# Performance work log

Measured on AMD Instinct MI355X. Metric: run time of the kernel, lower is better.

The kernel has to match this reference:

```python
import jax, jax.numpy as jnp
import numpy as np

HIDDEN = 64
HALF = 32
VOCAB = 64
B, L = 256, 2048


def _l2norm(x):
    # matches torch F.normalize(dim=-1, eps=1e-12)
    return x / jnp.maximum(jnp.linalg.norm(x, axis=-1, keepdims=True), 1e-12)


def setup_inputs() -> dict:
    key = jax.random.key(0)
    ks = jax.random.split(key, 16)
    s = 0.02
    return {
        "seq": jax.random.randint(ks[0], (B, L), 0, VOCAB),
        "embed": jax.random.normal(ks[1], (VOCAB, HIDDEN), jnp.float32) * s,
        "W1": jax.random.normal(ks[2], (2 * HIDDEN, HIDDEN), jnp.float32) * s,
        "b1": jnp.zeros((2 * HIDDEN,), jnp.float32),
        "W2": jax.random.normal(ks[3], (HIDDEN, 2 * HIDDEN), jnp.float32) * s,
        "b2": jnp.zeros((HIDDEN,), jnp.float32),
        "ln_g": jnp.ones((HIDDEN,), jnp.float32),
        "ln_b": jnp.zeros((HIDDEN,), jnp.float32),
        "Ws": jax.random.normal(ks[4], (HALF, HIDDEN), jnp.float32) * s,
        "bs": jnp.zeros((HALF,), jnp.float32),
        "We": jax.random.normal(ks[5], (HALF, HIDDEN), jnp.float32) * s,
        "be": jnp.zeros((HALF,), jnp.float32),
        "Wrp": jax.random.normal(ks[6], (HIDDEN, 2 * HALF), jnp.float32) * s,
        "brp": jnp.zeros((HIDDEN,), jnp.float32),
        "Wo": jax.random.normal(ks[7], (VOCAB, HIDDEN), jnp.float32) * s,
        "bo": jnp.zeros((VOCAB,), jnp.float32),
    }


def reference(seq, embed, W1, b1, W2, b2, ln_g, ln_b, Ws, bs, We, be, Wrp, brp, Wo, bo):
    # Encoder: embed -> LayerNorm(h + FF(h))
    h0 = embed[seq]                                     # [B,L,H]
    ff = jnp.maximum(h0 @ W1.T + b1, 0.0) @ W2.T + b2
    x = h0 + ff
    mu = x.mean(-1, keepdims=True)
    var = x.var(-1, keepdims=True)
    h = (x - mu) / jnp.sqrt(var + 1e-5) * ln_g + ln_b   # [B,L,H]

    Bn, Ln, _ = h.shape
    half = Ws.shape[0]
    hs_all = h @ Ws.T + bs                              # [B,L,half]
    he_all = h @ We.T + be

    # sequential delta-rule memory writes over t = 0 .. L-2
    hs_seq = jnp.swapaxes(hs_all[:, :-1], 0, 1)         # [L-1,B,half]
    he_seq = jnp.swapaxes(he_all[:, :-1], 0, 1)
    scales = (jnp.arange(1, Ln) / Ln).astype(h.dtype)   # (t+1)/L
    M0 = jnp.zeros((Bn, half, half), h.dtype)

    def step(carry, inp):
        M_s, M_e = carry
        hs, he, sc = inp
        ks_ = _l2norm(hs)
        ke_ = _l2norm(he)
        vps = jnp.einsum('bij,bj->bi', M_s, ks_)
        vpe = jnp.einsum('bij,bj->bi', M_e, ke_)
        M_s = M_s + (hs - vps)[:, :, None] * ks_[:, None, :]
        M_e = M_e + sc * (he - vpe)[:, :, None] * ke_[:, None, :]
        return (M_s, M_e), None

    (M_s, M_e), _ = jax.lax.scan(step, (M0, M0), (hs_seq, he_seq, scales))

    # read with last-position query
    qs = _l2norm(hs_all[:, -1])
    qe = _l2norm(he_all[:, -1])
    rs = jnp.einsum('bij,bj->bi', M_s, qs)
    re = jnp.einsum('bij,bj->bi', M_e, qe)
    r = jnp.concatenate([rs, re], axis=-1)              # [B, 2*half]
    return (r @ Wrp.T + brp) @ Wo.T + bo                # [B, vocab]
```

## Files before the change

### kernel.cpp

```cpp
#include <hip/hip_runtime.h>

#define HIDDEN 64
#define HALFD  32
#define VOCAB  64
#define BATCH  256
#define SEQLEN 2048
#define GPAD   65

#define RLF(v, sl) __int_as_float(__builtin_amdgcn_readlane(__float_as_int(v), (sl)))
#define RFL(x)     __builtin_amdgcn_readfirstlane(x)

__global__ __launch_bounds__(64) void vocab_kernel(
    const float* __restrict__ embed, const float* __restrict__ W1, const float* __restrict__ b1,
    const float* __restrict__ W2, const float* __restrict__ b2,
    const float* __restrict__ ln_g, const float* __restrict__ ln_b,
    const float* __restrict__ Ws, const float* __restrict__ bs,
    const float* __restrict__ We, const float* __restrict__ be,
    float* __restrict__ ws)
{
    const int v = blockIdx.x;
    const int tid = threadIdx.x;

    __shared__ float e_s[64];
    __shared__ float a1_s[128];
    __shared__ float h_s[64];

    e_s[tid] = embed[v * 64 + tid];
    __syncthreads();

    float acc0 = b1[tid], acc1 = b1[tid + 64];
    #pragma unroll 8
    for (int m = 0; m < 64; ++m) {
        float ev = e_s[m];
        acc0 = fmaf(ev, W1[tid * 64 + m], acc0);
        acc1 = fmaf(ev, W1[(tid + 64) * 64 + m], acc1);
    }
    a1_s[tid]      = fmaxf(acc0, 0.0f);
    a1_s[tid + 64] = fmaxf(acc1, 0.0f);
    __syncthreads();

    float ff = b2[tid];
    #pragma unroll 8
    for (int m = 0; m < 128; ++m) ff = fmaf(a1_s[m], W2[tid * 128 + m], ff);
    float x = e_s[tid] + ff;

    float s = x, s2 = x * x;
    #pragma unroll
    for (int off = 32; off >= 1; off >>= 1) {
        s  += __shfl_xor(s,  off, 64);
        s2 += __shfl_xor(s2, off, 64);
    }
    float mu  = s * (1.0f / 64.0f);
    float var = s2 * (1.0f / 64.0f) - mu * mu;
    float hval = (x - mu) * rsqrtf(var + 1e-5f) * ln_g[tid] + ln_b[tid];
    h_s[tid] = hval;
    __syncthreads();

    const int j = tid & 31;
    const bool is_s = tid < 32;
    const float* W = is_s ? Ws : We;
    float acc = is_s ? bs[j] : be[j];
    #pragma unroll 8
    for (int m = 0; m < 64; ++m) acc = fmaf(h_s[m], W[j * 64 + m], acc);

    float n2 = acc * acc;
    #pragma unroll
    for (int off = 16; off >= 1; off >>= 1) n2 += __shfl_xor(n2, off, 64);
    float norm = sqrtf(n2);
    float kn = acc / fmaxf(norm, 1e-12f);

    const int base = v * 32 + j;
    if (is_s) { ws[base]        = kn; ws[4096 + base] = acc; }
    else      { ws[2048 + base] = kn; ws[6144 + base] = acc; }
}

__global__ __launch_bounds__(256) void gram_kernel(float* __restrict__ ws)
{
    const int w = blockIdx.x;
    const int tid = threadIdx.x;
    __shared__ float k_s[2048];
    const float* kb = ws + w * 2048;
    for (int i = tid; i < 2048; i += 256) k_s[i] = kb[i];
    __syncthreads();
    const int a  = tid >> 2;
    const int b0 = (tid & 3) << 4;
    float* Gw = ws + 8192 + w * 4096 + a * 64;
    for (int bb = 0; bb < 16; ++bb) {
        const int bcol = b0 + bb;
        float acc = 0.f;
        #pragma unroll
        for (int m = 0; m < 32; ++m) acc = fmaf(k_s[a * 32 + m], k_s[bcol * 32 + m], acc);
        Gw[bcol] = acc;
    }
}

__global__ __launch_bounds__(128) void scan_kernel(
    const int* __restrict__ seq, const float* __restrict__ ws,
    const float* __restrict__ Wrp, const float* __restrict__ brp,
    const float* __restrict__ Wo, const float* __restrict__ bo,
    float* __restrict__ out)
{
    const int b    = blockIdx.x;
    const int tid  = threadIdx.x;
    const int w    = tid >> 6;
    const int lane = tid & 63;
    const bool is_e = (w == 1);

    __shared__ float Gl[2 * 64 * GPAD];
    __shared__ int   toklds[SEQLEN];
    __shared__ float wacc_s[2][64];
    __shared__ float r_s[64];
    __shared__ float t1_s[64];

    {
        const float4* gsrc = (const float4*)(ws + 8192);
        for (int i4 = tid; i4 < 2048; i4 += 128) {
            float4 gv = gsrc[i4];
            int idx = i4 << 2;
            int ww = idx >> 12, rc = idx & 4095;
            int rowi = rc >> 6, coli = rc & 63;
            float* d = &Gl[ww * (64 * GPAD) + rowi * GPAD + coli];
            d[0] = gv.x; d[1] = gv.y; d[2] = gv.z; d[3] = gv.w;
        }
        const int4* sq4 = (const int4*)(seq + b * SEQLEN);
        int4* tl4w = (int4*)toklds;
        #pragma unroll
        for (int i = 0; i < 4; ++i) tl4w[tid + i * 128] = sq4[tid + i * 128];
    }
    __syncthreads();

    const float* Gw = Gl + w * (64 * GPAD);
    const int4*  tl4 = (const int4*)toklds;

    const float invL = 1.0f / (float)SEQLEN;

    int4 tA  = tl4[510], tB  = tl4[511];
    int tk0 = RFL(tA.x), tk1 = RFL(tA.y), tk2 = RFL(tA.z), tk3 = RFL(tA.w);
    int tk4 = RFL(tB.x), tk5 = RFL(tB.y), tk6 = RFL(tB.z), tk7 = RFL(tB.w);
    int4 tA1 = tl4[508], tB1 = tl4[509];
    int nk0 = RFL(tA1.x), nk1 = RFL(tA1.y), nk2 = RFL(tA1.z), nk3 = RFL(tA1.w);
    int nk4 = RFL(tB1.x), nk5 = RFL(tB1.y), nk6 = RFL(tB1.z), nk7 = RFL(tB1.w);

    float grow0 = Gw[tk0 * GPAD + lane], grow1 = Gw[tk1 * GPAD + lane];
    float grow2 = Gw[tk2 * GPAD + lane], grow3 = Gw[tk3 * GPAD + lane];
    float grow4 = Gw[tk4 * GPAD + lane], grow5 = Gw[tk5 * GPAD + lane];
    float grow6 = Gw[tk6 * GPAD + lane], grow7 = Gw[tk7 * GPAD + lane];

    float u     = Gw[tk7 * GPAD + lane];
    float waccv = 0.0f;

    for (int c = 255; c >= 0; --c) {
        float t0 = __shfl(u, tk0, 64);
        float t1 = __shfl(u, tk1, 64);
        float t2 = __shfl(u, tk2, 64);
        float t3 = __shfl(u, tk3, 64);
        float t4 = __shfl(u, tk4, 64);
        float t5 = __shfl(u, tk5, 64);
        float t6 = __shfl(u, tk6, 64);
        float t7 = __shfl(u, tk7, 64);

        float g01 = RLF(grow0, tk1), g02 = RLF(grow0, tk2), g03 = RLF(grow0, tk3);
        float g04 = RLF(grow0, tk4), g05 = RLF(grow0, tk5), g06 = RLF(grow0, tk6), g07 = RLF(grow0, tk7);
        float g12 = RLF(grow1, tk2), g13 = RLF(grow1, tk3), g14 = RLF(grow1, tk4);
        float g15 = RLF(grow1, tk5), g16 = RLF(grow1, tk6), g17 = RLF(grow1, tk7);
        float g23 = RLF(grow2, tk3), g24 = RLF(grow2, tk4), g25 = RLF(grow2, tk5);
        float g26 = RLF(grow2, tk6), g27 = RLF(grow2, tk7);
        float g34 = RLF(grow3, tk4), g35 = RLF(grow3, tk5), g36 = RLF(grow3, tk6), g37 = RLF(grow3, tk7);
        float g45 = RLF(grow4, tk5), g46 = RLF(grow4, tk6), g47 = RLF(grow4, tk7);
        float g56 = RLF(grow5, tk6), g57 = RLF(grow5, tk7);
        float g67 = RLF(grow6, tk7);

        float gn0 = Gw[nk0 * GPAD + lane], gn1 = Gw[nk1 * GPAD + lane];
        float gn2 = Gw[nk2 * GPAD + lane], gn3 = Gw[nk3 * GPAD + lane];
        float gn4 = Gw[nk4 * GPAD + lane], gn5 = Gw[nk5 * GPAD + lane];
        float gn6 = Gw[nk6 * GPAD + lane], gn7 = Gw[nk7 * GPAD + lane];
        int cm2 = (c >= 2) ? (c - 2) : 0;
        int4 tA2 = tl4[cm2 * 2], tB2 = tl4[cm2 * 2 + 1];

        float fb = (float)(8 * c + 1) * invL;
        float f0 = is_e ? fb            : 1.0f;
        float f1 = is_e ? fb +     invL : 1.0f;
        float f2 = is_e ? fb + 2 * invL : 1.0f;
        float f3 = is_e ? fb + 3 * invL : 1.0f;
        float f4 = is_e ? fb + 4 * invL : 1.0f;
        float f5 = is_e ? fb + 5 * invL : 1.0f;
        float f6 = is_e ? fb + 6 * invL : 1.0f;
        float f7 = (c == 255) ? 0.0f : (is_e ? fb + 7 * invL : 1.0f);

        float s7 = f7 * t7;
        float s6 = f6 * (t6 - g67 * s7);
        float s5 = f5 * ((t5 - g57 * s7) - g56 * s6);
        float s4 = f4 * (((t4 - g47 * s7) - g46 * s6) - g45 * s5);
        float s3 = f3 * ((((t3 - g37 * s7) - g36 * s6) - g35 * s5) - g34 * s4);
        float s2 = f2 * (((((t2 - g27 * s7) - g26 * s6) - g25 * s5) - g24 * s4) - g23 * s3);
        float s1 = f1 * ((((((t1 - g17 * s7) - g16 * s6) - g15 * s5) - g14 * s4) - g13 * s3) - g12 * s2);
        float s0 = f0 * (((((((t0 - g07 * s7) - g06 * s6) - g05 * s5) - g04 * s4) - g03 * s3) - g02 * s2) - g01 * s1);

        {
            float A = fmaf(grow0, s0, fmaf(grow1, s1, fmaf(grow2, s2, grow3 * s3)));
            float B = fmaf(grow4, s4, fmaf(grow5, s5, fmaf(grow6, s6, grow7 * s7)));
            u -= (A + B);
        }

        waccv += (lane == tk0) ? s0 : 0.0f;
        waccv += (lane == tk1) ? s1 : 0.0f;
        waccv += (lane == tk2) ? s2 : 0.0f;
        waccv += (lane == tk3) ? s3 : 0.0f;
        waccv += (lane == tk4) ? s4 : 0.0f;
        waccv += (lane == tk5) ? s5 : 0.0f;
        waccv += (lane == tk6) ? s6 : 0.0f;
        waccv += (lane == tk7) ? s7 : 0.0f;

        tk0 = nk0; tk1 = nk1; tk2 = nk2; tk3 = nk3;
        tk4 = nk4; tk5 = nk5; tk6 = nk6; tk7 = nk7;
        nk0 = RFL(tA2.x); nk1 = RFL(tA2.y); nk2 = RFL(tA2.z); nk3 = RFL(tA2.w);
        nk4 = RFL(tB2.x); nk5 = RFL(tB2.y); nk6 = RFL(tB2.z); nk7 = RFL(tB2.w);
        grow0 = gn0; grow1 = gn1; grow2 = gn2; grow3 = gn3;
        grow4 = gn4; grow5 = gn5; grow6 = gn6; grow7 = gn7;
    }

    wacc_s[w][lane] = waccv;
    __syncthreads();

    if (tid < 64) {
        const int w2  = tid >> 5;
        const int rho = tid & 31;
        const float* vv = ws + 4096 + w2 * 2048;
        const float* wa = &wacc_s[w2][0];
        float acc = 0.0f;
        #pragma unroll 8
        for (int tok = 0; tok < 64; ++tok) acc = fmaf(wa[tok], vv[tok * 32 + rho], acc);
        r_s[tid] = acc;
    }
    __syncthreads();

    if (tid < 64) {
        float acc = brp[tid];
        #pragma unroll 8
        for (int m = 0; m < 64; ++m) acc = fmaf(Wrp[tid * 64 + m], r_s[m], acc);
        t1_s[tid] = acc;
    }
    __syncthreads();
    if (tid < 64) {
        float acc = bo[tid];
        #pragma unroll 8
        for (int m = 0; m < 64; ++m) acc = fmaf(Wo[tid * 64 + m], t1_s[m], acc);
        out[b * 64 + tid] = acc;
    }
}

extern "C" void kernel_launch(void* const* d_in, const int* in_sizes, int n_in,
                              void* d_out, int out_size, void* d_ws, size_t ws_size,
                              hipStream_t stream)
{
    const int*   seq   = (const int*)  d_in[0];
    const float* embed = (const float*)d_in[1];
    const float* W1    = (const float*)d_in[2];
    const float* b1    = (const float*)d_in[3];
    const float* W2    = (const float*)d_in[4];
    const float* b2    = (const float*)d_in[5];
    const float* ln_g  = (const float*)d_in[6];
    const float* ln_b  = (const float*)d_in[7];
    const float* Ws    = (const float*)d_in[8];
    const float* bs    = (const float*)d_in[9];
    const float* We    = (const float*)d_in[10];
    const float* be    = (const float*)d_in[11];
    const float* Wrp   = (const float*)d_in[12];
    const float* brp   = (const float*)d_in[13];
    const float* Wo    = (const float*)d_in[14];
    const float* bo    = (const float*)d_in[15];
    float* ws  = (float*)d_ws;
    float* out = (float*)d_out;

    hipLaunchKernelGGL(vocab_kernel, dim3(VOCAB), dim3(64), 0, stream,
                       embed, W1, b1, W2, b2, ln_g, ln_b, Ws, bs, We, be, ws);
    hipLaunchKernelGGL(gram_kernel, dim3(2), dim3(256), 0, stream, ws);
    hipLaunchKernelGGL(scan_kernel, dim3(BATCH), dim3(128), 0, stream,
                       seq, ws, Wrp, brp, Wo, bo, out);
}
```

Measured before the change: 230.2 us.

## Read Gram table and tokens from global memory instead of staging in LDS

Drops the LDS staging of the two 64x64 Gram tables and the token sequence, along with the block barrier. The scan loop now gathers Gram rows directly from global memory (served by L1/L2) and loads eight tokens per step as a per-lane vector. The eight per-step shuffles are replaced by a single shuffle indexed by the lane's token, followed by eight readlanes. This removes the prologue copy and the shared-memory footprint, which may raise occupancy, but it puts global-memory latency on the per-step prefetch path.

```diff
diff --git a/kernel.cpp b/kernel.cpp
--- a/kernel.cpp
+++ b/kernel.cpp
@@ -5,10 +5,9 @@
 #define VOCAB  64
 #define BATCH  256
 #define SEQLEN 2048
-#define GPAD   65
 
 #define RLF(v, sl) __int_as_float(__builtin_amdgcn_readlane(__float_as_int(v), (sl)))
-#define RFL(x)     __builtin_amdgcn_readfirstlane(x)
+#define RLI(v, sl) __builtin_amdgcn_readlane((v), (sl))
 
 __global__ __launch_bounds__(64) void vocab_kernel(
     const float* __restrict__ embed, const float* __restrict__ W1, const float* __restrict__ b1,
@@ -104,60 +103,43 @@
     const int tid  = threadIdx.x;
     const int w    = tid >> 6;
     const int lane = tid & 63;
+    const int l7   = lane & 7;
     const bool is_e = (w == 1);
 
-    __shared__ float Gl[2 * 64 * GPAD];
-    __shared__ int   toklds[SEQLEN];
     __shared__ float wacc_s[2][64];
     __shared__ float r_s[64];
     __shared__ float t1_s[64];
 
-    {
-        const float4* gsrc = (const float4*)(ws + 8192);
-        for (int i4 = tid; i4 < 2048; i4 += 128) {
-            float4 gv = gsrc[i4];
-            int idx = i4 << 2;
-            int ww = idx >> 12, rc = idx & 4095;
-            int rowi = rc >> 6, coli = rc & 63;
-            float* d = &Gl[ww * (64 * GPAD) + rowi * GPAD + coli];
-            d[0] = gv.x; d[1] = gv.y; d[2] = gv.z; d[3] = gv.w;
-        }
-        const int4* sq4 = (const int4*)(seq + b * SEQLEN);
-        int4* tl4w = (int4*)toklds;
-        #pragma unroll
-        for (int i = 0; i < 4; ++i) tl4w[tid + i * 128] = sq4[tid + i * 128];
-    }
-    __syncthreads();
-
-    const float* Gw = Gl + w * (64 * GPAD);
-    const int4*  tl4 = (const int4*)toklds;
+    const int*   sq = seq + b * SEQLEN;
+    const float* Gg = ws + 8192 + w * 4096;
 
     const float invL = 1.0f / (float)SEQLEN;
 
-    int4 tA  = tl4[510], tB  = tl4[511];
-    int tk0 = RFL(tA.x), tk1 = RFL(tA.y), tk2 = RFL(tA.z), tk3 = RFL(tA.w);
-    int tk4 = RFL(tB.x), tk5 = RFL(tB.y), tk6 = RFL(tB.z), tk7 = RFL(tB.w);
-    int4 tA1 = tl4[508], tB1 = tl4[509];
-    int nk0 = RFL(tA1.x), nk1 = RFL(tA1.y), nk2 = RFL(tA1.z), nk3 = RFL(tA1.w);
-    int nk4 = RFL(tB1.x), nk5 = RFL(tB1.y), nk6 = RFL(tB1.z), nk7 = RFL(tB1.w);
-
-    float grow0 = Gw[tk0 * GPAD + lane], grow1 = Gw[tk1 * GPAD + lane];
-    float grow2 = Gw[tk2 * GPAD + lane], grow3 = Gw[tk3 * GPAD + lane];
-    float grow4 = Gw[tk4 * GPAD + lane], grow5 = Gw[tk5 * GPAD + lane];
-    float grow6 = Gw[tk6 * GPAD + lane], grow7 = Gw[tk7 * GPAD + lane];
-
-    float u     = Gw[tk7 * GPAD + lane];
+    int tokvC = sq[2040 + l7];
+    int tk0 = RLI(tokvC, 0), tk1 = RLI(tokvC, 1), tk2 = RLI(tokvC, 2), tk3 = RLI(tokvC, 3);
+    int tk4 = RLI(tokvC, 4), tk5 = RLI(tokvC, 5), tk6 = RLI(tokvC, 6), tk7 = RLI(tokvC, 7);
+
+    float grow0 = Gg[tk0 * 64 + lane], grow1 = Gg[tk1 * 64 + lane];
+    float grow2 = Gg[tk2 * 64 + lane], grow3 = Gg[tk3 * 64 + lane];
+    float grow4 = Gg[tk4 * 64 + lane], grow5 = Gg[tk5 * 64 + lane];
+    float grow6 = Gg[tk6 * 64 + lane], grow7 = Gg[tk7 * 64 + lane];
+
+    int tokvN = sq[2032 + l7];
+
+    float u = Gg[tk7 * 64 + lane];
     float waccv = 0.0f;
 
     for (int c = 255; c >= 0; --c) {
-        float t0 = __shfl(u, tk0, 64);
-        float t1 = __shfl(u, tk1, 64);
-        float t2 = __shfl(u, tk2, 64);
-        float t3 = __shfl(u, tk3, 64);
-        float t4 = __shfl(u, tk4, 64);
-        float t5 = __shfl(u, tk5, 64);
-        float t6 = __shfl(u, tk6, 64);
-        float t7 = __shfl(u, tk7, 64);
+        float bp = __shfl(u, tokvC, 64);
+
+        int nk0 = RLI(tokvN, 0), nk1 = RLI(tokvN, 1), nk2 = RLI(tokvN, 2), nk3 = RLI(tokvN, 3);
+        int nk4 = RLI(tokvN, 4), nk5 = RLI(tokvN, 5), nk6 = RLI(tokvN, 6), nk7 = RLI(tokvN, 7);
+        float gn0 = Gg[nk0 * 64 + lane], gn1 = Gg[nk1 * 64 + lane];
+        float gn2 = Gg[nk2 * 64 + lane], gn3 = Gg[nk3 * 64 + lane];
+        float gn4 = Gg[nk4 * 64 + lane], gn5 = Gg[nk5 * 64 + lane];
+        float gn6 = Gg[nk6 * 64 + lane], gn7 = Gg[nk7 * 64 + lane];
+        int cm2 = (c >= 2) ? (c - 2) : 0;
+        int tokv2 = sq[cm2 * 8 + l7];
 
         float g01 = RLF(grow0, tk1), g02 = RLF(grow0, tk2), g03 = RLF(grow0, tk3);
         float g04 = RLF(grow0, tk4), g05 = RLF(grow0, tk5), g06 = RLF(grow0, tk6), g07 = RLF(grow0, tk7);
@@ -170,12 +152,8 @@
         float g56 = RLF(grow5, tk6), g57 = RLF(grow5, tk7);
         float g67 = RLF(grow6, tk7);
 
-        float gn0 = Gw[nk0 * GPAD + lane], gn1 = Gw[nk1 * GPAD + lane];
-        float gn2 = Gw[nk2 * GPAD + lane], gn3 = Gw[nk3 * GPAD + lane];
-        float gn4 = Gw[nk4 * GPAD + lane], gn5 = Gw[nk5 * GPAD + lane];
-        float gn6 = Gw[nk6 * GPAD + lane], gn7 = Gw[nk7 * GPAD + lane];
-        int cm2 = (c >= 2) ? (c - 2) : 0;
-        int4 tA2 = tl4[cm2 * 2], tB2 = tl4[cm2 * 2 + 1];
+        float t0 = RLF(bp, 0), t1 = RLF(bp, 1), t2 = RLF(bp, 2), t3 = RLF(bp, 3);
+        float t4 = RLF(bp, 4), t5 = RLF(bp, 5), t6 = RLF(bp, 6), t7 = RLF(bp, 7);
 
         float fb = (float)(8 * c + 1) * invL;
         float f0 = is_e ? fb            : 1.0f;
@@ -213,10 +191,9 @@
 
         tk0 = nk0; tk1 = nk1; tk2 = nk2; tk3 = nk3;
         tk4 = nk4; tk5 = nk5; tk6 = nk6; tk7 = nk7;
-        nk0 = RFL(tA2.x); nk1 = RFL(tA2.y); nk2 = RFL(tA2.z); nk3 = RFL(tA2.w);
-        nk4 = RFL(tB2.x); nk5 = RFL(tB2.y); nk6 = RFL(tB2.z); nk7 = RFL(tB2.w);
         grow0 = gn0; grow1 = gn1; grow2 = gn2; grow3 = gn3;
         grow4 = gn4; grow5 = gn5; grow6 = gn6; grow7 = gn7;
+        tokvC = tokvN; tokvN = tokv2;
     }
 
     wacc_s[w][lane] = waccv;
```

Measured after the change: 233.2 us. No clear change (+1.3%).
